# Kernel tuning notes

Hardware: AMD Instinct MI355X
Metric: run time of the kernel (lower is better)

Reference implementation:

```python
import jax, jax.numpy as jnp
import numpy as np

NEG_SLOPE = 0.2  # PyG GATConv default leaky_relu slope


def _gat_layer(x, src, dst, W, a_src, a_dst, b, N, concat):
    # x: [N, F_in]; W: [F_in, H*C]; a_src/a_dst: [H, C]; b: [H*C] or [C]
    H, C = a_src.shape
    h = (x @ W).reshape(N, H, C)                      # [N, H, C]
    al_s = jnp.einsum('nhc,hc->nh', h, a_src)          # [N, H]
    al_d = jnp.einsum('nhc,hc->nh', h, a_dst)          # [N, H]
    e = jax.nn.leaky_relu(al_s[src] + al_d[dst], NEG_SLOPE)  # [E, H]
    # segment softmax over incoming edges of each dst node
    m = jax.ops.segment_max(e, dst, num_segments=N)    # [N, H]
    ex = jnp.exp(e - m[dst])                           # [E, H]
    denom = jax.ops.segment_sum(ex, dst, num_segments=N)
    attn = ex / denom[dst]                             # [E, H]
    msg = (h[src] * attn[:, :, None]).reshape(-1, H * C)  # [E, H*C]
    out = jax.ops.segment_sum(msg, dst, num_segments=N)   # [N, H*C]
    if concat:
        return out + b
    return out.reshape(N, H, C).mean(axis=1) + b


def setup_inputs() -> dict:
    key = jax.random.key(0)
    ks = jax.random.split(key, 20)
    N, E, D, C, H = 20000, 160000, 768, 128, 4
    HC = H * C  # 512
    def glorot(k, shape):
        fan = shape[0] + shape[-1]
        return jax.random.uniform(k, shape, jnp.float32, -1.0, 1.0) * np.sqrt(6.0 / fan)
    inp = {
        'x': jax.random.normal(ks[0], (N, D), jnp.float32),
        'edge_index': jax.random.randint(ks[1], (2, E), 0, N, jnp.int64),
        'W1': glorot(ks[2], (D, HC)),  'as1': glorot(ks[3], (H, C)), 'ad1': glorot(ks[4], (H, C)), 'b1': jnp.zeros((HC,), jnp.float32),
        'W2': glorot(ks[5], (HC, HC)), 'as2': glorot(ks[6], (H, C)), 'ad2': glorot(ks[7], (H, C)), 'b2': jnp.zeros((HC,), jnp.float32),
        'W3': glorot(ks[8], (HC, C)),  'as3': glorot(ks[9], (1, C)), 'ad3': glorot(ks[10], (1, C)), 'b3': jnp.zeros((C,), jnp.float32),
        'Ws1': glorot(ks[11], (C, C // 2)), 'bs1': jnp.zeros((C // 2,), jnp.float32),
        'Ws2': glorot(ks[12], (C // 2, 1)), 'bs2': jnp.zeros((1,), jnp.float32),
    }
    return inp


def reference(x, edge_index, W1, as1, ad1, b1, W2, as2, ad2, b2, W3, as3, ad3, b3, Ws1, bs1, Ws2, bs2):
    N = x.shape[0]
    loops = jnp.arange(N, dtype=edge_index.dtype)
    src = jnp.concatenate([edge_index[0], loops])  # add self-loops (PyG default)
    dst = jnp.concatenate([edge_index[1], loops])
    h = _gat_layer(x, src, dst, W1, as1, ad1, b1, N, concat=True)
    h = jax.nn.relu(h)  # dropout is identity in eval mode
    h = _gat_layer(h, src, dst, W2, as2, ad2, b2, N, concat=True)
    h = jax.nn.relu(h)
    h = _gat_layer(h, src, dst, W3, as3, ad3, b3, N, concat=False)
    # risk scoring head: Linear -> ReLU -> Linear -> Sigmoid
    s = jax.nn.relu(h @ Ws1 + bs1)
    return jax.nn.sigmoid(s @ Ws2 + bs2)  # [N, 1]
```

## Files before the change

kernel.cpp:

```cpp
#include <hip/hip_runtime.h>
#include <hip/hip_bf16.h>
#include <math.h>

#define NEG_SLOPE 0.2f

typedef __attribute__((ext_vector_type(8))) __bf16 bf16x8;
typedef __attribute__((ext_vector_type(4))) float f32x4;

__device__ inline float lrelu(float v) { return v > 0.f ? v : NEG_SLOPE * v; }

__device__ inline unsigned short f2bf(float f) {
    __hip_bfloat16 h = __float2bfloat16(f);
    return *reinterpret_cast<unsigned short*>(&h);
}
__device__ inline float bf_lo(unsigned u) { return __uint_as_float(u << 16); }
__device__ inline float bf_hi(unsigned u) { return __uint_as_float(u & 0xffff0000u); }

__device__ inline void transpose_one(const float* __restrict__ in,
                                     unsigned short* __restrict__ out,
                                     int K, int N, int idx) {
    if (idx >= K * N) return;
    int n = idx / K, k = idx % K;
    out[(size_t)n * K + k] = f2bf(in[(size_t)k * N + n]);
}

__global__ __launch_bounds__(256) void preproc_kernel(
    const float* __restrict__ x, unsigned short* __restrict__ xbf, int n4,
    const float* __restrict__ W1, unsigned short* __restrict__ W1t,
    const float* __restrict__ W2, unsigned short* __restrict__ W2t,
    const float* __restrict__ W3, unsigned short* __restrict__ W3t,
    const float* __restrict__ Ws1, unsigned short* __restrict__ Ws1t,
    const int* __restrict__ ei, int E, int N, int* __restrict__ deg,
    int c0, int c1, int c2, int c3, int c4,
    int D, int HC, int C) {
    int b = blockIdx.x;
    int t = threadIdx.x;
    if (b < c0) {
        int i = b * 256 + t;
        if (i < n4) {
            float4 v = reinterpret_cast<const float4*>(x)[i];
            ushort4 o;
            o.x = f2bf(v.x); o.y = f2bf(v.y); o.z = f2bf(v.z); o.w = f2bf(v.w);
            reinterpret_cast<ushort4*>(xbf)[i] = o;
        }
        return;
    }
    b -= c0;
    if (b < c1) { transpose_one(W1, W1t, D, HC, b * 256 + t); return; }
    b -= c1;
    if (b < c2) { transpose_one(W2, W2t, HC, HC, b * 256 + t); return; }
    b -= c2;
    if (b < c3) { transpose_one(W3, W3t, HC, C, b * 256 + t); return; }
    b -= c3;
    if (b < c4) { transpose_one(Ws1, Ws1t, 128, 64, b * 256 + t); return; }
    b -= c4;
    {
        int e = b * 256 + t;
        if (e < E + N) {
            int dst = (e < E) ? ei[E + e] : (e - E);
            atomicAdd(&deg[dst], 1);
        }
    }
}

__global__ void scan_kernel(const int* __restrict__ deg, int* __restrict__ off, int N) {
    __shared__ int sums[1024];
    int tid = threadIdx.x;
    int chunk = (N + 1023) / 1024;
    int start = tid * chunk;
    int end = start + chunk; if (end > N) end = N;
    int s = 0;
#pragma unroll 4
    for (int i = start; i < end && i < N; i++) s += deg[i];
    sums[tid] = s;
    __syncthreads();
    for (int d = 1; d < 1024; d <<= 1) {
        int v = 0;
        if (tid >= d) v = sums[tid - d];
        __syncthreads();
        if (tid >= d) sums[tid] += v;
        __syncthreads();
    }
    int prefix = (tid == 0) ? 0 : sums[tid - 1];
    int run = prefix;
#pragma unroll 4
    for (int i = start; i < end && i < N; i++) { off[i] = run; run += deg[i]; }
    if (tid == 1023) off[N] = sums[1023];
}

__global__ void scatter_kernel(const int* __restrict__ ei, int E, int N,
                               const int* __restrict__ off, int* __restrict__ cursor,
                               int* __restrict__ csr_src) {
    int e = blockIdx.x * blockDim.x + threadIdx.x;
    if (e >= E + N) return;
    int src, dst;
    if (e < E) { src = ei[e]; dst = ei[E + e]; }
    else       { src = dst = e - E; }
    int pos = off[dst] + atomicAdd(&cursor[dst], 1);
    csr_src[pos] = src;
}

template <int HEADS>
__global__ __launch_bounds__(256) void gemm_bf16_alpha(const unsigned short* __restrict__ A,
                                                       const unsigned short* __restrict__ Bt,
                                                       unsigned short* __restrict__ C,
                                                       int M, int N, int K, int rowTiles,
                                                       const float* __restrict__ a_src,
                                                       const float* __restrict__ a_dst,
                                                       float* __restrict__ alS,
                                                       float* __restrict__ alD) {
    __shared__ unsigned short Asl[64 * 64];
    __shared__ unsigned short Bsl[128 * 64];
    const int tid  = threadIdx.x;
    const int lane = tid & 63;
    const int wave = tid >> 6;

    int r, c;
    {
        int b = blockIdx.x;
        int colTiles = N >> 7;
        if (colTiles == 4) {
            int mainRows = rowTiles & ~7;
            int mainBlocks = mainRows * 4;
            if (b < mainBlocks) {
                int xcd = b & 7;
                c = (b >> 3) & 3;
                r = (b >> 5) * 8 + xcd;
            } else {
                int idx = b - mainBlocks;
                r = mainRows + (idx >> 2);
                c = idx & 3;
            }
        } else { r = b; c = 0; }
    }
    const int rowBase = r * 64;
    const int colBase = c * 128;
    const int wm = (wave & 1) * 32;
    const int wn = (wave >> 1) * 64;
    const int q   = lane >> 4;
    const int l16 = lane & 15;

    const int r0 = tid >> 3;
    const int cg = (tid & 7) ^ (r0 & 7);

    f32x4 acc[2][4] = {};

    for (int k0 = 0; k0 < K; k0 += 64) {
#pragma unroll
        for (int it = 0; it < 2; it++) {
            int s = it * 256 + tid;
            int rr = it * 32 + r0;
            int ga = rowBase + rr; if (ga >= M) ga = M - 1;
            const unsigned short* gpa = A + (size_t)ga * K + k0 + cg * 8;
            __builtin_amdgcn_global_load_lds(
                (const __attribute__((address_space(1))) void*)gpa,
                (__attribute__((address_space(3))) void*)&Asl[(size_t)s * 8],
                16, 0, 0);
        }
#pragma unroll
        for (int it = 0; it < 4; it++) {
            int s = it * 256 + tid;
            int rr = it * 32 + r0;
            const unsigned short* gpb = Bt + (size_t)(colBase + rr) * K + k0 + cg * 8;
            __builtin_amdgcn_global_load_lds(
                (const __attribute__((address_space(1))) void*)gpb,
                (__attribute__((address_space(3))) void*)&Bsl[(size_t)s * 8],
                16, 0, 0);
        }
        __syncthreads();

#pragma unroll
        for (int kh = 0; kh < 2; kh++) {
            bf16x8 af[2], bfv[4];
#pragma unroll
            for (int mi = 0; mi < 2; mi++) {
                int row = wm + mi * 16 + l16;
                int ch = (kh * 4 + q) ^ (row & 7);
                af[mi] = *reinterpret_cast<const bf16x8*>(&Asl[row * 64 + ch * 8]);
            }
#pragma unroll
            for (int ni = 0; ni < 4; ni++) {
                int row = wn + ni * 16 + l16;
                int ch = (kh * 4 + q) ^ (row & 7);
                bfv[ni] = *reinterpret_cast<const bf16x8*>(&Bsl[row * 64 + ch * 8]);
            }
#pragma unroll
            for (int mi = 0; mi < 2; mi++)
#pragma unroll
                for (int ni = 0; ni < 4; ni++)
                    acc[mi][ni] = __builtin_amdgcn_mfma_f32_16x16x32_bf16(af[mi], bfv[ni], acc[mi][ni], 0, 0, 0);
        }
        __syncthreads();
    }

    const int hIdx = colBase >> 7;
    const float* asl = a_src + hIdx * 128;
    const float* adl = a_dst + hIdx * 128;
    float acoef[4], dcoef[4];
#pragma unroll
    for (int ni = 0; ni < 4; ni++) {
        int cl = wn + ni * 16 + l16;
        acoef[ni] = asl[cl];
        dcoef[ni] = adl[cl];
    }

    float2* red = reinterpret_cast<float2*>(Asl);
    const int half = wn >> 6;

#pragma unroll
    for (int mi = 0; mi < 2; mi++) {
#pragma unroll
        for (int rr = 0; rr < 4; rr++) {
            int lrow = wm + mi * 16 + q * 4 + rr;
            int grow = rowBase + lrow;
            bool ok = grow < M;
            float vs = 0.f, vd = 0.f;
#pragma unroll
            for (int ni = 0; ni < 4; ni++) {
                float hv = acc[mi][ni][rr];
                vs += hv * acoef[ni];
                vd += hv * dcoef[ni];
                if (ok) {
                    int gcol = colBase + wn + ni * 16 + l16;
                    C[(size_t)grow * N + gcol] = f2bf(hv);
                }
            }
#pragma unroll
            for (int d = 1; d < 16; d <<= 1) {
                vs += __shfl_xor(vs, d);
                vd += __shfl_xor(vd, d);
            }
            if (l16 == 0) red[lrow * 2 + half] = make_float2(vs, vd);
        }
    }
    __syncthreads();
    if (tid < 64) {
        int grow = rowBase + tid;
        if (grow < M) {
            float2 a = red[tid * 2 + 0];
            float2 b = red[tid * 2 + 1];
            alS[(size_t)grow * HEADS + hIdx] = a.x + b.x;
            alD[(size_t)grow * HEADS + hIdx] = a.y + b.y;
        }
    }
}

template <int H, int C, int MODE>
__global__ __launch_bounds__(256) void gat_aggregate(const unsigned short* __restrict__ hb,
                                                     const float* __restrict__ alS,
                                                     const float* __restrict__ alD,
                                                     const int* __restrict__ off,
                                                     const int* __restrict__ csr_src,
                                                     const float* __restrict__ bias,
                                                     unsigned short* __restrict__ outbuf,
                                                     int N) {
    constexpr int HC = H * C;
    constexpr int PER = HC / 64;
    __shared__ int   sIdx[4][16];
    __shared__ float sW[4][64];

    int n = (blockIdx.x * blockDim.x + threadIdx.x) >> 6;
    int lane = threadIdx.x & 63;
    int wave = threadIdx.x >> 6;
    if (n >= N) return;
    int beg = off[n], end = off[n + 1];

    const int grp  = lane >> 4;
    const int slot = lane & 15;
    const int myh  = (H == 4) ? grp : 0;
    const float adh = alD[n * H + myh];
    const unsigned short* hbl = hb + (size_t)lane * PER;
    const float* sWrow = &sW[wave][grp * 16];

    float m = -1e30f, dn = 0.f;
    float acc0 = 0.f, acc1 = 0.f, acc2 = 0.f, acc3 = 0.f,
          acc4 = 0.f, acc5 = 0.f, acc6 = 0.f, acc7 = 0.f;

    for (int base = beg; base < end; base += 16) {
        int cnt = end - base; if (cnt > 16) cnt = 16;
        bool act = slot < cnt;
        int s_l = csr_src[act ? (base + slot) : base];
        float v = act ? lrelu(alS[s_l * H + myh] + adh) : -1e30f;

        float mc = v;
#pragma unroll
        for (int d = 1; d < 16; d <<= 1) mc = fmaxf(mc, __shfl_xor(mc, d));
        float pl = __expf(v - mc);
        float dc = pl;
#pragma unroll
        for (int d = 1; d < 16; d <<= 1) dc += __shfl_xor(dc, d);
        float nm = fmaxf(m, mc);
        float so = __expf(m - nm);
        float sc = __expf(mc - nm);
        dn = dn * so + dc * sc;
        m = nm;
        float wl = pl * sc;

        if (lane < 16) sIdx[wave][lane] = s_l;
        sW[wave][lane] = wl;

        acc0 *= so; acc1 *= so;
        if (PER == 8) {
            acc2 *= so; acc3 *= so; acc4 *= so; acc5 *= so;
            acc6 *= so; acc7 *= so;
        }

        int cntR = (cnt + 3) & ~3;

        if (PER == 8) {
            int4   sI = *reinterpret_cast<const int4*>(&sIdx[wave][0]);
            float4 wv = *reinterpret_cast<const float4*>(&sWrow[0]);
            uint4 gA0 = *reinterpret_cast<const uint4*>(hbl + (size_t)sI.x * HC);
            uint4 gA1 = *reinterpret_cast<const uint4*>(hbl + (size_t)sI.y * HC);
            uint4 gA2 = *reinterpret_cast<const uint4*>(hbl + (size_t)sI.z * HC);
            uint4 gA3 = *reinterpret_cast<const uint4*>(hbl + (size_t)sI.w * HC);
            for (int i = 0; i < cntR; i += 4) {
                int4 sI2 = {}; float4 wv2 = {};
                uint4 gB0 = {}, gB1 = {}, gB2 = {}, gB3 = {};
                if (i + 4 < cntR) {
                    sI2 = *reinterpret_cast<const int4*>(&sIdx[wave][i + 4]);
                    wv2 = *reinterpret_cast<const float4*>(&sWrow[i + 4]);
                    gB0 = *reinterpret_cast<const uint4*>(hbl + (size_t)sI2.x * HC);
                    gB1 = *reinterpret_cast<const uint4*>(hbl + (size_t)sI2.y * HC);
                    gB2 = *reinterpret_cast<const uint4*>(hbl + (size_t)sI2.z * HC);
                    gB3 = *reinterpret_cast<const uint4*>(hbl + (size_t)sI2.w * HC);
                }
#define CONSUME(G, W)                                                   \
                { uint4 rc = G; float w = W;                            \
                  acc0 += bf_lo(rc.x) * w; acc1 += bf_hi(rc.x) * w;     \
                  acc2 += bf_lo(rc.y) * w; acc3 += bf_hi(rc.y) * w;     \
                  acc4 += bf_lo(rc.z) * w; acc5 += bf_hi(rc.z) * w;     \
                  acc6 += bf_lo(rc.w) * w; acc7 += bf_hi(rc.w) * w; }
                CONSUME(gA0, wv.x); CONSUME(gA1, wv.y);
                CONSUME(gA2, wv.z); CONSUME(gA3, wv.w);
#undef CONSUME
                sI = sI2; wv = wv2;
                gA0 = gB0; gA1 = gB1; gA2 = gB2; gA3 = gB3;
            }
        } else {
            int4   sI = *reinterpret_cast<const int4*>(&sIdx[wave][0]);
            float4 wv = *reinterpret_cast<const float4*>(&sWrow[0]);
            unsigned gA0 = *reinterpret_cast<const unsigned*>(hbl + (size_t)sI.x * HC);
            unsigned gA1 = *reinterpret_cast<const unsigned*>(hbl + (size_t)sI.y * HC);
            unsigned gA2 = *reinterpret_cast<const unsigned*>(hbl + (size_t)sI.z * HC);
            unsigned gA3 = *reinterpret_cast<const unsigned*>(hbl + (size_t)sI.w * HC);
            for (int i = 0; i < cntR; i += 4) {
                int4 sI2 = {}; float4 wv2 = {};
                unsigned gB0 = 0, gB1 = 0, gB2 = 0, gB3 = 0;
                if (i + 4 < cntR) {
                    sI2 = *reinterpret_cast<const int4*>(&sIdx[wave][i + 4]);
                    wv2 = *reinterpret_cast<const float4*>(&sWrow[i + 4]);
                    gB0 = *reinterpret_cast<const unsigned*>(hbl + (size_t)sI2.x * HC);
                    gB1 = *reinterpret_cast<const unsigned*>(hbl + (size_t)sI2.y * HC);
                    gB2 = *reinterpret_cast<const unsigned*>(hbl + (size_t)sI2.z * HC);
                    gB3 = *reinterpret_cast<const unsigned*>(hbl + (size_t)sI2.w * HC);
                }
                acc0 += bf_lo(gA0) * wv.x; acc1 += bf_hi(gA0) * wv.x;
                acc0 += bf_lo(gA1) * wv.y; acc1 += bf_hi(gA1) * wv.y;
                acc0 += bf_lo(gA2) * wv.z; acc1 += bf_hi(gA2) * wv.z;
                acc0 += bf_lo(gA3) * wv.w; acc1 += bf_hi(gA3) * wv.w;
                sI = sI2; wv = wv2;
                gA0 = gB0; gA1 = gB1; gA2 = gB2; gA3 = gB3;
            }
        }
    }

    float invd = 1.f / dn;
    unsigned short* op = outbuf + (size_t)n * HC + lane * PER;
    const float* bp = bias + lane * PER;
    if (PER == 8) {
        float o0 = acc0 * invd + bp[0], o1 = acc1 * invd + bp[1];
        float o2 = acc2 * invd + bp[2], o3 = acc3 * invd + bp[3];
        float o4 = acc4 * invd + bp[4], o5 = acc5 * invd + bp[5];
        float o6 = acc6 * invd + bp[6], o7 = acc7 * invd + bp[7];
        if (MODE == 0) {
            o0 = fmaxf(o0, 0.f); o1 = fmaxf(o1, 0.f); o2 = fmaxf(o2, 0.f); o3 = fmaxf(o3, 0.f);
            o4 = fmaxf(o4, 0.f); o5 = fmaxf(o5, 0.f); o6 = fmaxf(o6, 0.f); o7 = fmaxf(o7, 0.f);
        }
        op[0] = f2bf(o0); op[1] = f2bf(o1); op[2] = f2bf(o2); op[3] = f2bf(o3);
        op[4] = f2bf(o4); op[5] = f2bf(o5); op[6] = f2bf(o6); op[7] = f2bf(o7);
    } else {
        float o0 = acc0 * invd + bp[0], o1 = acc1 * invd + bp[1];
        if (MODE == 0) { o0 = fmaxf(o0, 0.f); o1 = fmaxf(o1, 0.f); }
        op[0] = f2bf(o0); op[1] = f2bf(o1);
    }
}

__global__ __launch_bounds__(256) void head_mfma(const unsigned short* __restrict__ H3,
                                                 const unsigned short* __restrict__ W1t,
                                                 const float* __restrict__ bs1,
                                                 const float* __restrict__ Ws2,
                                                 const float* __restrict__ bs2,
                                                 float* __restrict__ out, int M) {
    __shared__ unsigned short Asl[128 * 128];
    __shared__ unsigned short Bsl[64 * 128];
    const int tid = threadIdx.x, lane = tid & 63, wave = tid >> 6;
    const int q = lane >> 4, l16 = lane & 15;
    const int rowBase = blockIdx.x * 128;
    const int r0 = tid >> 4;
    const int cg = (tid & 15) ^ (r0 & 7);

#pragma unroll
    for (int it = 0; it < 8; it++) {
        int s = it * 256 + tid;
        int r = it * 16 + r0;
        int ga = rowBase + r; if (ga >= M) ga = M - 1;
        const unsigned short* gp = H3 + (size_t)ga * 128 + cg * 8;
        __builtin_amdgcn_global_load_lds(
            (const __attribute__((address_space(1))) void*)gp,
            (__attribute__((address_space(3))) void*)&Asl[(size_t)s * 8], 16, 0, 0);
    }
#pragma unroll
    for (int it = 0; it < 4; it++) {
        int s = it * 256 + tid;
        int r = it * 16 + r0;
        const unsigned short* gp = W1t + (size_t)r * 128 + cg * 8;
        __builtin_amdgcn_global_load_lds(
            (const __attribute__((address_space(1))) void*)gp,
            (__attribute__((address_space(3))) void*)&Bsl[(size_t)s * 8], 16, 0, 0);
    }
    __syncthreads();

    const int wm = wave * 32;
    f32x4 acc[2][4] = {};
#pragma unroll
    for (int kh = 0; kh < 4; kh++) {
        bf16x8 af[2], bfv[4];
#pragma unroll
        for (int mi = 0; mi < 2; mi++) {
            int row = wm + mi * 16 + l16;
            int ch = (kh * 4 + q) ^ (row & 7);
            af[mi] = *reinterpret_cast<const bf16x8*>(&Asl[row * 128 + ch * 8]);
        }
#pragma unroll
        for (int ni = 0; ni < 4; ni++) {
            int row = ni * 16 + l16;
            int ch = (kh * 4 + q) ^ (row & 7);
            bfv[ni] = *reinterpret_cast<const bf16x8*>(&Bsl[row * 128 + ch * 8]);
        }
#pragma unroll
        for (int mi = 0; mi < 2; mi++)
#pragma unroll
            for (int ni = 0; ni < 4; ni++)
                acc[mi][ni] = __builtin_amdgcn_mfma_f32_16x16x32_bf16(af[mi], bfv[ni], acc[mi][ni], 0, 0, 0);
    }
    __syncthreads();

    float b1v[4], w2v[4];
#pragma unroll
    for (int ni = 0; ni < 4; ni++) {
        int cI = ni * 16 + l16;
        b1v[ni] = bs1[cI];
        w2v[ni] = Ws2[cI];
    }
    float* red = reinterpret_cast<float*>(Bsl);
#pragma unroll
    for (int mi = 0; mi < 2; mi++) {
#pragma unroll
        for (int r = 0; r < 4; r++) {
            int lrow = wm + mi * 16 + q * 4 + r;
            float p = 0.f;
#pragma unroll
            for (int ni = 0; ni < 4; ni++)
                p += fmaxf(acc[mi][ni][r] + b1v[ni], 0.f) * w2v[ni];
#pragma unroll
            for (int d = 1; d < 16; d <<= 1) p += __shfl_xor(p, d);
            if (l16 == 0) red[lrow] = p;
        }
    }
    __syncthreads();
    if (tid < 128) {
        int g = rowBase + tid;
        if (g < M) out[g] = 1.f / (1.f + __expf(-(red[tid] + bs2[0])));
    }
}

extern "C" void kernel_launch(void* const* d_in, const int* in_sizes, int n_in,
                              void* d_out, int out_size, void* d_ws, size_t ws_size,
                              hipStream_t stream) {
    const float* x   = (const float*)d_in[0];
    const int*   ei  = (const int*)d_in[1];
    const float* W1  = (const float*)d_in[2];
    const float* as1 = (const float*)d_in[3];
    const float* ad1 = (const float*)d_in[4];
    const float* b1  = (const float*)d_in[5];
    const float* W2  = (const float*)d_in[6];
    const float* as2 = (const float*)d_in[7];
    const float* ad2 = (const float*)d_in[8];
    const float* b2  = (const float*)d_in[9];
    const float* W3  = (const float*)d_in[10];
    const float* as3 = (const float*)d_in[11];
    const float* ad3 = (const float*)d_in[12];
    const float* b3  = (const float*)d_in[13];
    const float* Ws1 = (const float*)d_in[14];
    const float* bs1 = (const float*)d_in[15];
    const float* Ws2 = (const float*)d_in[16];
    const float* bs2 = (const float*)d_in[17];

    const int N = out_size;
    const int E = in_sizes[1] / 2;
    const int D = in_sizes[0] / N;
    const int HC = 512, H = 4, C = 128;
    const int Etot = E + N;

    char* p = (char*)d_ws;
    auto alloc = [&](size_t bytes) -> void* {
        void* q = (void*)p;
        p += (bytes + 255) & ~(size_t)255;
        return q;
    };
    char*  zbeg   = p;
    int*   deg    = (int*)alloc((size_t)N * 4);
    int*   cursor = (int*)alloc((size_t)N * 4);
    char*  zend   = p;
    float* alS1   = (float*)alloc((size_t)N * H * 4);
    float* alD1   = (float*)alloc((size_t)N * H * 4);
    float* alS2   = (float*)alloc((size_t)N * H * 4);
    float* alD2   = (float*)alloc((size_t)N * H * 4);
    float* alS3   = (float*)alloc((size_t)N * 4);
    float* alD3   = (float*)alloc((size_t)N * 4);
    int*   off    = (int*)alloc((size_t)(N + 1) * 4);
    int*   csr    = (int*)alloc((size_t)Etot * 4);
    unsigned short* hbuf = (unsigned short*)alloc((size_t)N * HC * 2);
    unsigned short* xbf  = (unsigned short*)alloc((size_t)N * D * 2);
    unsigned short* obf  = (unsigned short*)alloc((size_t)N * HC * 2);
    unsigned short* W1t  = (unsigned short*)alloc((size_t)D * HC * 2);
    unsigned short* W2t  = (unsigned short*)alloc((size_t)HC * HC * 2);
    unsigned short* W3t  = (unsigned short*)alloc((size_t)HC * C * 2);
    unsigned short* Ws1t = (unsigned short*)alloc((size_t)C * 64 * 2);

    hipMemsetAsync(zbeg, 0, (size_t)(zend - zbeg), stream);

    {
        int n4 = N * D / 4;
        int c0 = (n4 + 255) / 256;
        int c1 = (D * HC + 255) / 256;
        int c2 = (HC * HC + 255) / 256;
        int c3 = (HC * C + 255) / 256;
        int c4 = (128 * 64 + 255) / 256;
        int c5 = (Etot + 255) / 256;
        int total = c0 + c1 + c2 + c3 + c4 + c5;
        preproc_kernel<<<total, 256, 0, stream>>>(
            x, xbf, n4, W1, W1t, W2, W2t, W3, W3t, Ws1, Ws1t,
            ei, E, N, deg, c0, c1, c2, c3, c4, D, HC, C);
    }
    scan_kernel<<<1, 1024, 0, stream>>>(deg, off, N);
    scatter_kernel<<<(Etot + 255) / 256, 256, 0, stream>>>(ei, E, N, off, cursor, csr);

    int node_blocks = (N + 3) / 4;
    int rowTiles64 = (N + 63) / 64;
    int headTiles = (N + 127) / 128;

    gemm_bf16_alpha<4><<<rowTiles64 * 4, 256, 0, stream>>>(
        xbf, W1t, hbuf, N, HC, D, rowTiles64, as1, ad1, alS1, alD1);
    gat_aggregate<4, 128, 0><<<node_blocks, 256, 0, stream>>>(
        hbuf, alS1, alD1, off, csr, b1, obf, N);

    gemm_bf16_alpha<4><<<rowTiles64 * 4, 256, 0, stream>>>(
        obf, W2t, hbuf, N, HC, HC, rowTiles64, as2, ad2, alS2, alD2);
    gat_aggregate<4, 128, 0><<<node_blocks, 256, 0, stream>>>(
        hbuf, alS2, alD2, off, csr, b2, obf, N);

    gemm_bf16_alpha<1><<<rowTiles64, 256, 0, stream>>>(
        obf, W3t, hbuf, N, C, HC, rowTiles64, as3, ad3, alS3, alD3);
    gat_aggregate<1, 128, 2><<<node_blocks, 256, 0, stream>>>(
        hbuf, alS3, alD3, off, csr, b3, xbf, N);

    head_mfma<<<headTiles, 256, 0, stream>>>(xbf, Ws1t, bs1, Ws2, bs2, (float*)d_out, N);
}
```

Before: 298.7 us.

## Fuse x fp32-to-bf16 conversion into first GEMM and widen GEMM tiles to 256 columns

Removes the separate conversion pass that wrote a bf16 copy of x (20000x768), so the first GEMM now reads fp32 x directly and converts to bf16 while staging into LDS. Layers 1 and 2 switch to a new GEMM with 64x256 tiles (two heads per block), which halves the number of column tiles and therefore how many times A is reread. The cost is more accumulator registers per thread and more LDS per block, which may lower occupancy. The fp32 A path also uses ordinary register loads instead of direct global-to-LDS loads.

```diff
diff --git a/kernel.cpp b/kernel.cpp
--- a/kernel.cpp
+++ b/kernel.cpp
@@ -25,27 +25,15 @@
 }
 
 __global__ __launch_bounds__(256) void preproc_kernel(
-    const float* __restrict__ x, unsigned short* __restrict__ xbf, int n4,
     const float* __restrict__ W1, unsigned short* __restrict__ W1t,
     const float* __restrict__ W2, unsigned short* __restrict__ W2t,
     const float* __restrict__ W3, unsigned short* __restrict__ W3t,
     const float* __restrict__ Ws1, unsigned short* __restrict__ Ws1t,
     const int* __restrict__ ei, int E, int N, int* __restrict__ deg,
-    int c0, int c1, int c2, int c3, int c4,
+    int c1, int c2, int c3, int c4,
     int D, int HC, int C) {
     int b = blockIdx.x;
     int t = threadIdx.x;
-    if (b < c0) {
-        int i = b * 256 + t;
-        if (i < n4) {
-            float4 v = reinterpret_cast<const float4*>(x)[i];
-            ushort4 o;
-            o.x = f2bf(v.x); o.y = f2bf(v.y); o.z = f2bf(v.z); o.w = f2bf(v.w);
-            reinterpret_cast<ushort4*>(xbf)[i] = o;
-        }
-        return;
-    }
-    b -= c0;
     if (b < c1) { transpose_one(W1, W1t, D, HC, b * 256 + t); return; }
     b -= c1;
     if (b < c2) { transpose_one(W2, W2t, HC, HC, b * 256 + t); return; }
@@ -100,6 +88,167 @@
     csr_src[pos] = src;
 }
 
+template <int HEADS, bool AFP32>
+__global__ __launch_bounds__(256) void gemm256(const void* __restrict__ Araw,
+                                               const unsigned short* __restrict__ Bt,
+                                               unsigned short* __restrict__ Cc,
+                                               int M, int N, int K, int rowTiles,
+                                               const float* __restrict__ a_src,
+                                               const float* __restrict__ a_dst,
+                                               float* __restrict__ alS,
+                                               float* __restrict__ alD) {
+    __shared__ unsigned short Asl[64 * 64];
+    __shared__ unsigned short Bsl[256 * 64];
+    const int tid  = threadIdx.x;
+    const int lane = tid & 63;
+    const int wave = tid >> 6;
+
+    int r, c;
+    {
+        int b = blockIdx.x;
+        int mainRows = rowTiles & ~7;
+        int mainBlocks = mainRows * 2;
+        if (b < mainBlocks) {
+            int xcd = b & 7;
+            c = (b >> 3) & 1;
+            r = (b >> 4) * 8 + xcd;
+        } else {
+            int idx = b - mainBlocks;
+            r = mainRows + (idx >> 1);
+            c = idx & 1;
+        }
+    }
+    const int rowBase = r * 64;
+    const int colBase = c * 256;
+    const int wm = (wave & 1) * 32;
+    const int wn = (wave >> 1) * 128;
+    const int q   = lane >> 4;
+    const int l16 = lane & 15;
+
+    const int r0 = tid >> 3;
+    const int cg = (tid & 7) ^ (r0 & 7);
+
+    f32x4 acc[2][8] = {};
+
+    for (int k0 = 0; k0 < K; k0 += 64) {
+        if (AFP32) {
+            const float* Af = (const float*)Araw;
+#pragma unroll
+            for (int it = 0; it < 2; it++) {
+                int row = it * 32 + r0;
+                int ga = rowBase + row; if (ga >= M) ga = M - 1;
+                const float* gp = Af + (size_t)ga * K + k0 + (tid & 7) * 8;
+                float4 v0 = *reinterpret_cast<const float4*>(gp);
+                float4 v1 = *reinterpret_cast<const float4*>(gp + 4);
+                ushort4 o0, o1;
+                o0.x = f2bf(v0.x); o0.y = f2bf(v0.y); o0.z = f2bf(v0.z); o0.w = f2bf(v0.w);
+                o1.x = f2bf(v1.x); o1.y = f2bf(v1.y); o1.z = f2bf(v1.z); o1.w = f2bf(v1.w);
+                int sc = (tid & 7) ^ (row & 7);
+                ushort4* dp = reinterpret_cast<ushort4*>(&Asl[row * 64 + sc * 8]);
+                dp[0] = o0; dp[1] = o1;
+            }
+        } else {
+            const unsigned short* Ab = (const unsigned short*)Araw;
+#pragma unroll
+            for (int it = 0; it < 2; it++) {
+                int s = it * 256 + tid;
+                int rr = it * 32 + r0;
+                int ga = rowBase + rr; if (ga >= M) ga = M - 1;
+                const unsigned short* gpa = Ab + (size_t)ga * K + k0 + cg * 8;
+                __builtin_amdgcn_global_load_lds(
+                    (const __attribute__((address_space(1))) void*)gpa,
+                    (__attribute__((address_space(3))) void*)&Asl[(size_t)s * 8],
+                    16, 0, 0);
+            }
+        }
+#pragma unroll
+        for (int it = 0; it < 8; it++) {
+            int s = it * 256 + tid;
+            int rr = it * 32 + r0;
+            const unsigned short* gpb = Bt + (size_t)(colBase + rr) * K + k0 + cg * 8;
+            __builtin_amdgcn_global_load_lds(
+                (const __attribute__((address_space(1))) void*)gpb,
+                (__attribute__((address_space(3))) void*)&Bsl[(size_t)s * 8],
+                16, 0, 0);
+        }
+        __syncthreads();
+
+#pragma unroll
+        for (int kh = 0; kh < 2; kh++) {
+            bf16x8 af[2], bfv[8];
+#pragma unroll
+            for (int mi = 0; mi < 2; mi++) {
+                int row = wm + mi * 16 + l16;
+                int ch = (kh * 4 + q) ^ (row & 7);
+                af[mi] = *reinterpret_cast<const bf16x8*>(&Asl[row * 64 + ch * 8]);
+            }
+#pragma unroll
+            for (int ni = 0; ni < 8; ni++) {
+                int row = wn + ni * 16 + l16;
+                int ch = (kh * 4 + q) ^ (row & 7);
+                bfv[ni] = *reinterpret_cast<const bf16x8*>(&Bsl[row * 64 + ch * 8]);
+            }
+#pragma unroll
+            for (int mi = 0; mi < 2; mi++)
+#pragma unroll
+                for (int ni = 0; ni < 8; ni++)
+                    acc[mi][ni] = __builtin_amdgcn_mfma_f32_16x16x32_bf16(af[mi], bfv[ni], acc[mi][ni], 0, 0, 0);
+        }
+        __syncthreads();
+    }
+
+    const int hIdx = (colBase + wn) >> 7;
+    const int hl   = wn >> 7;
+    const float* aslp = a_src + hIdx * 128;
+    const float* adlp = a_dst + hIdx * 128;
+    float acoef[8], dcoef[8];
+#pragma unroll
+    for (int ni = 0; ni < 8; ni++) {
+        int cl = ni * 16 + l16;
+        acoef[ni] = aslp[cl];
+        dcoef[ni] = adlp[cl];
+    }
+
+    float2* red = reinterpret_cast<float2*>(Asl);
+
+#pragma unroll
+    for (int mi = 0; mi < 2; mi++) {
+#pragma unroll
+        for (int rr = 0; rr < 4; rr++) {
+            int lrow = wm + mi * 16 + q * 4 + rr;
+            int grow = rowBase + lrow;
+            bool ok = grow < M;
+            float vs = 0.f, vd = 0.f;
+#pragma unroll
+            for (int ni = 0; ni < 8; ni++) {
+                float hv = acc[mi][ni][rr];
+                vs += hv * acoef[ni];
+                vd += hv * dcoef[ni];
+                if (ok) {
+                    int gcol = colBase + wn + ni * 16 + l16;
+                    Cc[(size_t)grow * N + gcol] = f2bf(hv);
+                }
+            }
+#pragma unroll
+            for (int d = 1; d < 16; d <<= 1) {
+                vs += __shfl_xor(vs, d);
+                vd += __shfl_xor(vd, d);
+            }
+            if (l16 == 0) red[lrow * 2 + hl] = make_float2(vs, vd);
+        }
+    }
+    __syncthreads();
+    if (tid < 128) {
+        int row = tid & 63, hh = tid >> 6;
+        int grow = rowBase + row;
+        if (grow < M) {
+            float2 v = red[row * 2 + hh];
+            alS[(size_t)grow * HEADS + (colBase >> 7) + hh] = v.x;
+            alD[(size_t)grow * HEADS + (colBase >> 7) + hh] = v.y;
+        }
+    }
+}
+
 template <int HEADS>
 __global__ __launch_bounds__(256) void gemm_bf16_alpha(const unsigned short* __restrict__ A,
                                                        const unsigned short* __restrict__ Bt,
@@ -115,24 +264,7 @@
     const int lane = tid & 63;
     const int wave = tid >> 6;
 
-    int r, c;
-    {
-        int b = blockIdx.x;
-        int colTiles = N >> 7;
-        if (colTiles == 4) {
-            int mainRows = rowTiles & ~7;
-            int mainBlocks = mainRows * 4;
-            if (b < mainBlocks) {
-                int xcd = b & 7;
-                c = (b >> 3) & 3;
-                r = (b >> 5) * 8 + xcd;
-            } else {
-                int idx = b - mainBlocks;
-                r = mainRows + (idx >> 2);
-                c = idx & 3;
-            }
-        } else { r = b; c = 0; }
-    }
+    int r = blockIdx.x, c = 0;
     const int rowBase = r * 64;
     const int colBase = c * 128;
     const int wm = (wave & 1) * 32;
@@ -522,7 +654,7 @@
     int*   off    = (int*)alloc((size_t)(N + 1) * 4);
     int*   csr    = (int*)alloc((size_t)Etot * 4);
     unsigned short* hbuf = (unsigned short*)alloc((size_t)N * HC * 2);
-    unsigned short* xbf  = (unsigned short*)alloc((size_t)N * D * 2);
+    unsigned short* h3bf = (unsigned short*)alloc((size_t)N * C * 2);
     unsigned short* obf  = (unsigned short*)alloc((size_t)N * HC * 2);
     unsigned short* W1t  = (unsigned short*)alloc((size_t)D * HC * 2);
     unsigned short* W2t  = (unsigned short*)alloc((size_t)HC * HC * 2);
@@ -532,17 +664,15 @@
     hipMemsetAsync(zbeg, 0, (size_t)(zend - zbeg), stream);
 
     {
-        int n4 = N * D / 4;
-        int c0 = (n4 + 255) / 256;
         int c1 = (D * HC + 255) / 256;
         int c2 = (HC * HC + 255) / 256;
         int c3 = (HC * C + 255) / 256;
         int c4 = (128 * 64 + 255) / 256;
         int c5 = (Etot + 255) / 256;
-        int total = c0 + c1 + c2 + c3 + c4 + c5;
+        int total = c1 + c2 + c3 + c4 + c5;
         preproc_kernel<<<total, 256, 0, stream>>>(
-            x, xbf, n4, W1, W1t, W2, W2t, W3, W3t, Ws1, Ws1t,
-            ei, E, N, deg, c0, c1, c2, c3, c4, D, HC, C);
+            W1, W1t, W2, W2t, W3, W3t, Ws1, Ws1t,
+            ei, E, N, deg, c1, c2, c3, c4, D, HC, C);
     }
     scan_kernel<<<1, 1024, 0, stream>>>(deg, off, N);
     scatter_kernel<<<(Etot + 255) / 256, 256, 0, stream>>>(ei, E, N, off, cursor, csr);
@@ -551,20 +681,20 @@
     int rowTiles64 = (N + 63) / 64;
     int headTiles = (N + 127) / 128;
 
-    gemm_bf16_alpha<4><<<rowTiles64 * 4, 256, 0, stream>>>(
-        xbf, W1t, hbuf, N, HC, D, rowTiles64, as1, ad1, alS1, alD1);
+    gemm256<4, true><<<rowTiles64 * 2, 256, 0, stream>>>(
+        (const void*)x, W1t, hbuf, N, HC, D, rowTiles64, as1, ad1, alS1, alD1);
     gat_aggregate<4, 128, 0><<<node_blocks, 256, 0, stream>>>(
         hbuf, alS1, alD1, off, csr, b1, obf, N);
 
-    gemm_bf16_alpha<4><<<rowTiles64 * 4, 256, 0, stream>>>(
-        obf, W2t, hbuf, N, HC, HC, rowTiles64, as2, ad2, alS2, alD2);
+    gemm256<4, false><<<rowTiles64 * 2, 256, 0, stream>>>(
+        (const void*)obf, W2t, hbuf, N, HC, HC, rowTiles64, as2, ad2, alS2, alD2);
     gat_aggregate<4, 128, 0><<<node_blocks, 256, 0, stream>>>(
         hbuf, alS2, alD2, off, csr, b2, obf, N);
 
     gemm_bf16_alpha<1><<<rowTiles64, 256, 0, stream>>>(
         obf, W3t, hbuf, N, C, HC, rowTiles64, as3, ad3, alS3, alD3);
     gat_aggregate<1, 128, 2><<<node_blocks, 256, 0, stream>>>(
-        hbuf, alS3, alD3, off, csr, b3, xbf, N);
-
-    head_mfma<<<headTiles, 256, 0, stream>>>(xbf, Ws1t, bs1, Ws2, bs2, (float*)d_out, N);
-}
+        hbuf, alS3, alD3, off, csr, b3, h3bf, N);
+
+    head_mfma<<<headTiles, 256, 0, stream>>>(h3bf, Ws1t, bs1, Ws2, bs2, (float*)d_out, N);
+}
```

Result: slower. 313.7 us (+5.0%).

## Double-buffer GEMM K loop with larger 128x256 tiles and 512-thread blocks

Applied to the files above, without the earlier changes.

Replaces the single-buffered 64x128 GEMM with a 128x256 tile, 512-thread kernel. It uses two LDS buffers of 32-wide K slices and explicit vmcnt/barrier waits, so global-to-LDS loads for the next slice overlap MFMA on the current one. Layer 3 gets its own double-buffered 64x128 kernel, and the layer-3 output now goes to a separate buffer instead of reusing xbf. The changes target load latency stalls and improve operand reuse per block, but they cut the number of blocks to about 314 and raise register pressure through 16 accumulators per wave.

```diff
diff --git a/kernel.cpp b/kernel.cpp
--- a/kernel.cpp
+++ b/kernel.cpp
@@ -15,6 +15,12 @@
 }
 __device__ inline float bf_lo(unsigned u) { return __uint_as_float(u << 16); }
 __device__ inline float bf_hi(unsigned u) { return __uint_as_float(u & 0xffff0000u); }
+
+__device__ inline void gld16(const unsigned short* gp, unsigned short* lp) {
+    __builtin_amdgcn_global_load_lds(
+        (const __attribute__((address_space(1))) void*)gp,
+        (__attribute__((address_space(3))) void*)lp, 16, 0, 0);
+}
 
 __device__ inline void transpose_one(const float* __restrict__ in,
                                      unsigned short* __restrict__ out,
@@ -23,6 +29,11 @@
     int n = idx / K, k = idx % K;
     out[(size_t)n * K + k] = f2bf(in[(size_t)k * N + n]);
 }
+
+#define BARRIER()    asm volatile("s_barrier" ::: "memory")
+#define WAIT_LGKM0() asm volatile("s_waitcnt lgkmcnt(0)" ::: "memory")
+#define WAIT_VM0()   asm volatile("s_waitcnt vmcnt(0)" ::: "memory")
+#define WAIT_VM3()   asm volatile("s_waitcnt vmcnt(3)" ::: "memory")
 
 __global__ __launch_bounds__(256) void preproc_kernel(
     const float* __restrict__ x, unsigned short* __restrict__ xbf, int n4,
@@ -101,16 +112,16 @@
 }
 
 template <int HEADS>
-__global__ __launch_bounds__(256) void gemm_bf16_alpha(const unsigned short* __restrict__ A,
-                                                       const unsigned short* __restrict__ Bt,
-                                                       unsigned short* __restrict__ C,
-                                                       int M, int N, int K, int rowTiles,
-                                                       const float* __restrict__ a_src,
-                                                       const float* __restrict__ a_dst,
-                                                       float* __restrict__ alS,
-                                                       float* __restrict__ alD) {
-    __shared__ unsigned short Asl[64 * 64];
-    __shared__ unsigned short Bsl[128 * 64];
+__global__ __launch_bounds__(512) void gemm_big(const unsigned short* __restrict__ A,
+                                                const unsigned short* __restrict__ Bt,
+                                                unsigned short* __restrict__ Cc,
+                                                int M, int N, int K, int rowTiles,
+                                                const float* __restrict__ a_src,
+                                                const float* __restrict__ a_dst,
+                                                float* __restrict__ alS,
+                                                float* __restrict__ alD) {
+    __shared__ unsigned short Asl[2][128 * 32];
+    __shared__ unsigned short Bsl[2][256 * 32];
     const int tid  = threadIdx.x;
     const int lane = tid & 63;
     const int wave = tid >> 6;
@@ -118,97 +129,103 @@
     int r, c;
     {
         int b = blockIdx.x;
-        int colTiles = N >> 7;
-        if (colTiles == 4) {
-            int mainRows = rowTiles & ~7;
-            int mainBlocks = mainRows * 4;
-            if (b < mainBlocks) {
-                int xcd = b & 7;
-                c = (b >> 3) & 3;
-                r = (b >> 5) * 8 + xcd;
-            } else {
-                int idx = b - mainBlocks;
-                r = mainRows + (idx >> 2);
-                c = idx & 3;
-            }
-        } else { r = b; c = 0; }
-    }
-    const int rowBase = r * 64;
-    const int colBase = c * 128;
-    const int wm = (wave & 1) * 32;
+        int mainRows = rowTiles & ~7;
+        int mainBlocks = mainRows * 2;
+        if (b < mainBlocks) {
+            int xcd = b & 7;
+            c = (b >> 3) & 1;
+            r = (b >> 4) * 8 + xcd;
+        } else {
+            int idx = b - mainBlocks;
+            r = mainRows + (idx >> 1);
+            c = idx & 1;
+        }
+    }
+    const int rowBase = r * 128;
+    const int colBase = c * 256;
+    const int wm = (wave & 1) * 64;
     const int wn = (wave >> 1) * 64;
     const int q   = lane >> 4;
     const int l16 = lane & 15;
 
-    const int r0 = tid >> 3;
-    const int cg = (tid & 7) ^ (r0 & 7);
-
-    f32x4 acc[2][4] = {};
-
-    for (int k0 = 0; k0 < K; k0 += 64) {
-#pragma unroll
-        for (int it = 0; it < 2; it++) {
-            int s = it * 256 + tid;
-            int rr = it * 32 + r0;
-            int ga = rowBase + rr; if (ga >= M) ga = M - 1;
-            const unsigned short* gpa = A + (size_t)ga * K + k0 + cg * 8;
-            __builtin_amdgcn_global_load_lds(
-                (const __attribute__((address_space(1))) void*)gpa,
-                (__attribute__((address_space(3))) void*)&Asl[(size_t)s * 8],
-                16, 0, 0);
-        }
-#pragma unroll
-        for (int it = 0; it < 4; it++) {
-            int s = it * 256 + tid;
-            int rr = it * 32 + r0;
-            const unsigned short* gpb = Bt + (size_t)(colBase + rr) * K + k0 + cg * 8;
-            __builtin_amdgcn_global_load_lds(
-                (const __attribute__((address_space(1))) void*)gpb,
-                (__attribute__((address_space(3))) void*)&Bsl[(size_t)s * 8],
-                16, 0, 0);
-        }
-        __syncthreads();
-
-#pragma unroll
-        for (int kh = 0; kh < 2; kh++) {
-            bf16x8 af[2], bfv[4];
-#pragma unroll
-            for (int mi = 0; mi < 2; mi++) {
-                int row = wm + mi * 16 + l16;
-                int ch = (kh * 4 + q) ^ (row & 7);
-                af[mi] = *reinterpret_cast<const bf16x8*>(&Asl[row * 64 + ch * 8]);
-            }
-#pragma unroll
-            for (int ni = 0; ni < 4; ni++) {
-                int row = wn + ni * 16 + l16;
-                int ch = (kh * 4 + q) ^ (row & 7);
-                bfv[ni] = *reinterpret_cast<const bf16x8*>(&Bsl[row * 64 + ch * 8]);
-            }
-#pragma unroll
-            for (int mi = 0; mi < 2; mi++)
-#pragma unroll
-                for (int ni = 0; ni < 4; ni++)
-                    acc[mi][ni] = __builtin_amdgcn_mfma_f32_16x16x32_bf16(af[mi], bfv[ni], acc[mi][ni], 0, 0, 0);
-        }
-        __syncthreads();
-    }
-
-    const int hIdx = colBase >> 7;
-    const float* asl = a_src + hIdx * 128;
-    const float* adl = a_dst + hIdx * 128;
+    const int ar  = tid >> 2;
+    const int acg = (tid & 3) ^ ((ar >> 1) & 3);
+    int gaA = rowBase + ar; if (gaA >= M) gaA = M - 1;
+    const unsigned short* gpA0 = A + (size_t)gaA * K + acg * 8;
+
+    const int br0  = tid >> 2;
+    const int bcg0 = (tid & 3) ^ ((br0 >> 1) & 3);
+    const int br1  = (tid + 512) >> 2;
+    const int bcg1 = (tid & 3) ^ ((br1 >> 1) & 3);
+    const unsigned short* gpB0 = Bt + (size_t)(colBase + br0) * K + bcg0 * 8;
+    const unsigned short* gpB1 = Bt + (size_t)(colBase + br1) * K + bcg1 * 8;
+
+    const int nk = K >> 5;
+    f32x4 acc[4][4] = {};
+
+    auto stage = [&](int kt, int buf) {
+        gld16(gpA0 + kt * 32, &Asl[buf][tid * 8]);
+        gld16(gpB0 + kt * 32, &Bsl[buf][tid * 8]);
+        gld16(gpB1 + kt * 32, &Bsl[buf][(size_t)(tid + 512) * 8]);
+    };
+    auto compute = [&](int buf) {
+        bf16x8 af[4], bfv[4];
+#pragma unroll
+        for (int mi = 0; mi < 4; mi++) {
+            int row = wm + mi * 16 + l16;
+            int ch = q ^ ((row >> 1) & 3);
+            af[mi] = *reinterpret_cast<const bf16x8*>(&Asl[buf][row * 32 + ch * 8]);
+        }
+#pragma unroll
+        for (int ni = 0; ni < 4; ni++) {
+            int row = wn + ni * 16 + l16;
+            int ch = q ^ ((row >> 1) & 3);
+            bfv[ni] = *reinterpret_cast<const bf16x8*>(&Bsl[buf][row * 32 + ch * 8]);
+        }
+#pragma unroll
+        for (int mi = 0; mi < 4; mi++)
+#pragma unroll
+            for (int ni = 0; ni < 4; ni++)
+                acc[mi][ni] = __builtin_amdgcn_mfma_f32_16x16x32_bf16(af[mi], bfv[ni], acc[mi][ni], 0, 0, 0);
+    };
+
+    stage(0, 0);
+    for (int kt = 0; kt < nk; kt += 2) {
+        stage(kt + 1, 1);
+        WAIT_VM3();
+        BARRIER();
+        compute(0);
+        WAIT_LGKM0();
+        BARRIER();
+        if (kt + 2 < nk) {
+            stage(kt + 2, 0);
+            WAIT_VM3();
+        } else {
+            WAIT_VM0();
+        }
+        BARRIER();
+        compute(1);
+        WAIT_LGKM0();
+        BARRIER();
+    }
+
+    const int headBase = colBase >> 7;
+    const int hl   = wn >> 7;
+    const int half = (wn >> 6) & 1;
+    const float* aslp = a_src + (headBase + hl) * 128;
+    const float* adlp = a_dst + (headBase + hl) * 128;
     float acoef[4], dcoef[4];
 #pragma unroll
     for (int ni = 0; ni < 4; ni++) {
-        int cl = wn + ni * 16 + l16;
-        acoef[ni] = asl[cl];
-        dcoef[ni] = adl[cl];
-    }
-
-    float2* red = reinterpret_cast<float2*>(Asl);
-    const int half = wn >> 6;
-
-#pragma unroll
-    for (int mi = 0; mi < 2; mi++) {
+        int cl = half * 64 + ni * 16 + l16;
+        acoef[ni] = aslp[cl];
+        dcoef[ni] = adlp[cl];
+    }
+
+    float2* red = reinterpret_cast<float2*>(&Asl[0][0]);
+
+#pragma unroll
+    for (int mi = 0; mi < 4; mi++) {
 #pragma unroll
         for (int rr = 0; rr < 4; rr++) {
             int lrow = wm + mi * 16 + q * 4 + rr;
@@ -222,7 +239,138 @@
                 vd += hv * dcoef[ni];
                 if (ok) {
                     int gcol = colBase + wn + ni * 16 + l16;
-                    C[(size_t)grow * N + gcol] = f2bf(hv);
+                    Cc[(size_t)grow * N + gcol] = f2bf(hv);
+                }
+            }
+#pragma unroll
+            for (int d = 1; d < 16; d <<= 1) {
+                vs += __shfl_xor(vs, d);
+                vd += __shfl_xor(vd, d);
+            }
+            if (l16 == 0) red[lrow * 4 + hl * 2 + half] = make_float2(vs, vd);
+        }
+    }
+    __syncthreads();
+    if (tid < 256) {
+        int row = tid >> 1, hh = tid & 1;
+        int grow = rowBase + row;
+        if (grow < M) {
+            float2 a = red[row * 4 + hh * 2 + 0];
+            float2 b = red[row * 4 + hh * 2 + 1];
+            alS[(size_t)grow * HEADS + headBase + hh] = a.x + b.x;
+            alD[(size_t)grow * HEADS + headBase + hh] = a.y + b.y;
+        }
+    }
+}
+
+__global__ __launch_bounds__(256) void gemm_l3(const unsigned short* __restrict__ A,
+                                               const unsigned short* __restrict__ Bt,
+                                               unsigned short* __restrict__ Cc,
+                                               int M, int K,
+                                               const float* __restrict__ a_src,
+                                               const float* __restrict__ a_dst,
+                                               float* __restrict__ alS,
+                                               float* __restrict__ alD) {
+    const int N = 128;
+    __shared__ unsigned short Asl[2][64 * 32];
+    __shared__ unsigned short Bsl[2][128 * 32];
+    const int tid  = threadIdx.x;
+    const int lane = tid & 63;
+    const int wave = tid >> 6;
+    const int rowBase = blockIdx.x * 64;
+    const int wm = (wave & 1) * 32;
+    const int wn = (wave >> 1) * 64;
+    const int q   = lane >> 4;
+    const int l16 = lane & 15;
+
+    const int ar  = tid >> 2;
+    const int acg = (tid & 3) ^ ((ar >> 1) & 3);
+    int gaA = rowBase + ar; if (gaA >= M) gaA = M - 1;
+    const unsigned short* gpA0 = A + (size_t)gaA * K + acg * 8;
+
+    const int br0  = tid >> 2;
+    const int bcg0 = (tid & 3) ^ ((br0 >> 1) & 3);
+    const int br1  = (tid + 256) >> 2;
+    const int bcg1 = (tid & 3) ^ ((br1 >> 1) & 3);
+    const unsigned short* gpB0 = Bt + (size_t)br0 * K + bcg0 * 8;
+    const unsigned short* gpB1 = Bt + (size_t)br1 * K + bcg1 * 8;
+
+    const int nk = K >> 5;
+    f32x4 acc[2][4] = {};
+
+    auto stage = [&](int kt, int buf) {
+        gld16(gpA0 + kt * 32, &Asl[buf][tid * 8]);
+        gld16(gpB0 + kt * 32, &Bsl[buf][tid * 8]);
+        gld16(gpB1 + kt * 32, &Bsl[buf][(size_t)(tid + 256) * 8]);
+    };
+    auto compute = [&](int buf) {
+        bf16x8 af[2], bfv[4];
+#pragma unroll
+        for (int mi = 0; mi < 2; mi++) {
+            int row = wm + mi * 16 + l16;
+            int ch = q ^ ((row >> 1) & 3);
+            af[mi] = *reinterpret_cast<const bf16x8*>(&Asl[buf][row * 32 + ch * 8]);
+        }
+#pragma unroll
+        for (int ni = 0; ni < 4; ni++) {
+            int row = wn + ni * 16 + l16;
+            int ch = q ^ ((row >> 1) & 3);
+            bfv[ni] = *reinterpret_cast<const bf16x8*>(&Bsl[buf][row * 32 + ch * 8]);
+        }
+#pragma unroll
+        for (int mi = 0; mi < 2; mi++)
+#pragma unroll
+            for (int ni = 0; ni < 4; ni++)
+                acc[mi][ni] = __builtin_amdgcn_mfma_f32_16x16x32_bf16(af[mi], bfv[ni], acc[mi][ni], 0, 0, 0);
+    };
+
+    stage(0, 0);
+    for (int kt = 0; kt < nk; kt += 2) {
+        stage(kt + 1, 1);
+        WAIT_VM3();
+        BARRIER();
+        compute(0);
+        WAIT_LGKM0();
+        BARRIER();
+        if (kt + 2 < nk) {
+            stage(kt + 2, 0);
+            WAIT_VM3();
+        } else {
+            WAIT_VM0();
+        }
+        BARRIER();
+        compute(1);
+        WAIT_LGKM0();
+        BARRIER();
+    }
+
+    const int half = wn >> 6;
+    float acoef[4], dcoef[4];
+#pragma unroll
+    for (int ni = 0; ni < 4; ni++) {
+        int cl = wn + ni * 16 + l16;
+        acoef[ni] = a_src[cl];
+        dcoef[ni] = a_dst[cl];
+    }
+
+    float2* red = reinterpret_cast<float2*>(&Asl[0][0]);
+
+#pragma unroll
+    for (int mi = 0; mi < 2; mi++) {
+#pragma unroll
+        for (int rr = 0; rr < 4; rr++) {
+            int lrow = wm + mi * 16 + q * 4 + rr;
+            int grow = rowBase + lrow;
+            bool ok = grow < M;
+            float vs = 0.f, vd = 0.f;
+#pragma unroll
+            for (int ni = 0; ni < 4; ni++) {
+                float hv = acc[mi][ni][rr];
+                vs += hv * acoef[ni];
+                vd += hv * dcoef[ni];
+                if (ok) {
+                    int gcol = wn + ni * 16 + l16;
+                    Cc[(size_t)grow * N + gcol] = f2bf(hv);
                 }
             }
 #pragma unroll
@@ -239,8 +387,8 @@
         if (grow < M) {
             float2 a = red[tid * 2 + 0];
             float2 b = red[tid * 2 + 1];
-            alS[(size_t)grow * HEADS + hIdx] = a.x + b.x;
-            alD[(size_t)grow * HEADS + hIdx] = a.y + b.y;
+            alS[grow] = a.x + b.x;
+            alD[grow] = a.y + b.y;
         }
     }
 }
@@ -406,18 +554,14 @@
         int r = it * 16 + r0;
         int ga = rowBase + r; if (ga >= M) ga = M - 1;
         const unsigned short* gp = H3 + (size_t)ga * 128 + cg * 8;
-        __builtin_amdgcn_global_load_lds(
-            (const __attribute__((address_space(1))) void*)gp,
-            (__attribute__((address_space(3))) void*)&Asl[(size_t)s * 8], 16, 0, 0);
+        gld16(gp, &Asl[(size_t)s * 8]);
     }
 #pragma unroll
     for (int it = 0; it < 4; it++) {
         int s = it * 256 + tid;
         int r = it * 16 + r0;
         const unsigned short* gp = W1t + (size_t)r * 128 + cg * 8;
-        __builtin_amdgcn_global_load_lds(
-            (const __attribute__((address_space(1))) void*)gp,
-            (__attribute__((address_space(3))) void*)&Bsl[(size_t)s * 8], 16, 0, 0);
+        gld16(gp, &Bsl[(size_t)s * 8]);
     }
     __syncthreads();
 
@@ -522,8 +666,9 @@
     int*   off    = (int*)alloc((size_t)(N + 1) * 4);
     int*   csr    = (int*)alloc((size_t)Etot * 4);
     unsigned short* hbuf = (unsigned short*)alloc((size_t)N * HC * 2);
+    unsigned short* h3bf = (unsigned short*)alloc((size_t)N * C * 2);
+    unsigned short* obf  = (unsigned short*)alloc((size_t)N * HC * 2);
     unsigned short* xbf  = (unsigned short*)alloc((size_t)N * D * 2);
-    unsigned short* obf  = (unsigned short*)alloc((size_t)N * HC * 2);
     unsigned short* W1t  = (unsigned short*)alloc((size_t)D * HC * 2);
     unsigned short* W2t  = (unsigned short*)alloc((size_t)HC * HC * 2);
     unsigned short* W3t  = (unsigned short*)alloc((size_t)HC * C * 2);
@@ -548,23 +693,24 @@
     scatter_kernel<<<(Etot + 255) / 256, 256, 0, stream>>>(ei, E, N, off, cursor, csr);
 
     int node_blocks = (N + 3) / 4;
-    int rowTiles64 = (N + 63) / 64;
-    int headTiles = (N + 127) / 128;
-
-    gemm_bf16_alpha<4><<<rowTiles64 * 4, 256, 0, stream>>>(
-        xbf, W1t, hbuf, N, HC, D, rowTiles64, as1, ad1, alS1, alD1);
+    int rowTiles128 = (N + 127) / 128;
+    int rowTiles64  = (N + 63) / 64;
+    int headTiles   = (N + 127) / 128;
+
+    gemm_big<4><<<rowTiles128 * 2, 512, 0, stream>>>(
+        xbf, W1t, hbuf, N, HC, D, rowTiles128, as1, ad1, alS1, alD1);
     gat_aggregate<4, 128, 0><<<node_blocks, 256, 0, stream>>>(
         hbuf, alS1, alD1, off, csr, b1, obf, N);
 
-    gemm_bf16_alpha<4><<<rowTiles64 * 4, 256, 0, stream>>>(
-        obf, W2t, hbuf, N, HC, HC, rowTiles64, as2, ad2, alS2, alD2);
+    gemm_big<4><<<rowTiles128 * 2, 512, 0, stream>>>(
+        obf, W2t, hbuf, N, HC, HC, rowTiles128, as2, ad2, alS2, alD2);
     gat_aggregate<4, 128, 0><<<node_blocks, 256, 0, stream>>>(
         hbuf, alS2, alD2, off, csr, b2, obf, N);
 
-    gemm_bf16_alpha<1><<<rowTiles64, 256, 0, stream>>>(
-        obf, W3t, hbuf, N, C, HC, rowTiles64, as3, ad3, alS3, alD3);
+    gemm_l3<<<rowTiles64, 256, 0, stream>>>(
+        obf, W3t, hbuf, N, HC, as3, ad3, alS3, alD3);
     gat_aggregate<1, 128, 2><<<node_blocks, 256, 0, stream>>>(
-        hbuf, alS3, alD3, off, csr, b3, xbf, N);
-
-    head_mfma<<<headTiles, 256, 0, stream>>>(xbf, Ws1t, bs1, Ws2, bs2, (float*)d_out, N);
-}
+        hbuf, alS3, alD3, off, csr, b3, h3bf, N);
+
+    head_mfma<<<headTiles, 256, 0, stream>>>(h3bf, Ws1t, bs1, Ws2, bs2, (float*)d_out, N);
+}
```

After: 304.4 us. No clear change (+1.9%).
